# Kernel optimization log

Measured on AMD Instinct MI355X. Metric: run time of the kernel, lower is better.

Reference implementation:

```python
import jax, jax.numpy as jnp
import numpy as np

NUM_ITEMS = 200000
EMBED_DIM = 128
EPS = 1e-8  # torch cosine_similarity eps
TEMP = 0.1


def setup_inputs() -> dict:
    key = jax.random.key(0)
    k1, k2, k3, k4, k5, k6, k7, k8 = jax.random.split(key, 8)
    g1 = jax.random.normal(k1, (NUM_ITEMS, EMBED_DIM), dtype=jnp.float32)
    g2 = jax.random.normal(k2, (NUM_ITEMS, EMBED_DIM), dtype=jnp.float32)
    s1 = jax.random.normal(k3, (NUM_ITEMS, EMBED_DIM), dtype=jnp.float32)
    s2 = jax.random.normal(k4, (NUM_ITEMS, EMBED_DIM), dtype=jnp.float32)
    att_w = jax.random.normal(k5, (2 * EMBED_DIM,), dtype=jnp.float32)
    idx = jnp.arange(NUM_ITEMS, dtype=jnp.int32)
    # negative index != i, uniform over remaining items (matches resample loop)
    def neg(k):
        off = jax.random.randint(k, (NUM_ITEMS,), 1, NUM_ITEMS, dtype=jnp.int32)
        return (idx + off) % NUM_ITEMS
    return {
        "g_emb_1": g1, "g_emb_2": g2, "s_emb_1": s1, "s_emb_2": s2,
        "att_w": att_w,
        "neg_graph": neg(k6), "neg_seq": neg(k7), "neg_cross": neg(k8),
    }


def _cos(a, b):
    # rowwise cosine similarity with torch-style eps clamp on norm product
    num = jnp.sum(a * b, axis=-1)
    na = jnp.linalg.norm(a, axis=-1)
    nb = jnp.linalg.norm(b, axis=-1)
    return num / jnp.maximum(na * nb, EPS)


def _info_nce(e1, e2, neg_idx, temperature=TEMP):
    pos = _cos(e1, e2)                 # [N]
    neg = _cos(e1, e2[neg_idx])        # [N]
    # -log(exp(p/t)/(exp(p/t)+exp(n/t))) == softplus((n-p)/t)
    return jnp.mean(jax.nn.softplus((neg - pos) / temperature))


def reference(g_emb_1, g_emb_2, s_emb_1, s_emb_2, att_w,
              neg_graph, neg_seq, neg_cross):
    L_graph = _info_nce(g_emb_1, g_emb_2, neg_graph)
    L_seq = _info_nce(s_emb_1, s_emb_2, neg_seq)
    g_avg = 0.5 * (g_emb_1 + g_emb_2)
    s_avg = 0.5 * (s_emb_1 + s_emb_2)
    L_cross = _info_nce(g_avg, s_avg, neg_cross)
    L_CL = L_graph + L_seq + 1.0 * L_cross  # cross_weight = 1.0
    combined = jnp.concatenate([g_avg, s_avg], axis=1)  # [N, 2D]
    alpha = jax.nn.sigmoid(combined @ att_w)[:, None]   # [N, 1]
    item_embeddings = alpha * g_avg + (1.0 - alpha) * s_avg
    return item_embeddings, L_CL
```

## Files before the change

kernel.cpp:

```cpp
#include <hip/hip_runtime.h>

#define N_ITEMS 200000
#define EPSV 1e-8f
#define INV_TEMP 10.0f

__device__ __forceinline__ float softplus_f(float x) {
    return fmaxf(x, 0.0f) + log1pf(expf(-fabsf(x)));
}

__device__ __forceinline__ float dot8(const float4& a0, const float4& a1,
                                      const float4& b0, const float4& b1) {
    return a0.x * b0.x + a0.y * b0.y + a0.z * b0.z + a0.w * b0.w +
           a1.x * b1.x + a1.y * b1.y + a1.z * b1.z + a1.w * b1.w;
}

__device__ __forceinline__ float4 avg4(const float4& a, const float4& b) {
    return make_float4(0.5f * (a.x + b.x), 0.5f * (a.y + b.y),
                       0.5f * (a.z + b.z), 0.5f * (a.w + b.w));
}

__global__ void mvr_init_ws(float* ws) {
    if (threadIdx.x < 3) ws[threadIdx.x] = 0.0f;
}

__global__ __launch_bounds__(256) void mvr_main(
    const float* __restrict__ g1, const float* __restrict__ g2,
    const float* __restrict__ s1, const float* __restrict__ s2,
    const float* __restrict__ att_w,
    const int* __restrict__ neg_g, const int* __restrict__ neg_s,
    const int* __restrict__ neg_c,
    float* __restrict__ out, float* __restrict__ loss_acc)
{
    const int tid = threadIdx.x;
    const int lane = tid & 63;
    const int g = lane >> 4;
    const int l = lane & 15;
    const int wavesPerBlock = blockDim.x >> 6;
    const int waveId = blockIdx.x * wavesPerBlock + (tid >> 6);
    const int waveStride = gridDim.x * wavesPerBlock;

    const float4* W = (const float4*)att_w;
    const float4 wa0 = W[l], wa1 = W[16 + l];
    const float4 wb0 = W[32 + l], wb1 = W[48 + l];

    const float4* G1p = (const float4*)g1;
    const float4* G2p = (const float4*)g2;
    const float4* S1p = (const float4*)s1;
    const float4* S2p = (const float4*)s2;
    float4* Op = (float4*)out;

    float accG = 0.0f, accS = 0.0f, accC = 0.0f;

    for (int base = waveId * 4; base < N_ITEMS; base += waveStride * 4) {
        const int item = base + g;
        const size_t rb = (size_t)item * 32;

        float4 G1a = G1p[rb + l], G1b = G1p[rb + 16 + l];
        float4 G2a = G2p[rb + l], G2b = G2p[rb + 16 + l];
        float4 S1a = S1p[rb + l], S1b = S1p[rb + 16 + l];
        float4 S2a = S2p[rb + l], S2b = S2p[rb + 16 + l];

        const int jg = neg_g[item];
        const int js = neg_s[item];
        const int jc = neg_c[item];
        const size_t rg = (size_t)jg * 32, rs = (size_t)js * 32, rc = (size_t)jc * 32;
        float4 Gna = G2p[rg + l], Gnb = G2p[rg + 16 + l];
        float4 Sna = S2p[rs + l], Snb = S2p[rs + 16 + l];
        float4 C1a = S1p[rc + l], C1b = S1p[rc + 16 + l];
        float4 C2a = S2p[rc + l], C2b = S2p[rc + 16 + l];

        float4 GAa = avg4(G1a, G2a), GAb = avg4(G1b, G2b);
        float4 SAa = avg4(S1a, S2a), SAb = avg4(S1b, S2b);
        float4 CNa = avg4(C1a, C2a), CNb = avg4(C1b, C2b);

        float v[16];
        v[0]  = dot8(G1a, G1b, G2a, G2b);
        v[1]  = dot8(G1a, G1b, G1a, G1b);
        v[2]  = dot8(G2a, G2b, G2a, G2b);
        v[3]  = dot8(G1a, G1b, Gna, Gnb);
        v[4]  = dot8(Gna, Gnb, Gna, Gnb);
        v[5]  = dot8(S1a, S1b, S2a, S2b);
        v[6]  = dot8(S1a, S1b, S1a, S1b);
        v[7]  = dot8(S2a, S2b, S2a, S2b);
        v[8]  = dot8(S1a, S1b, Sna, Snb);
        v[9]  = dot8(Sna, Snb, Sna, Snb);
        v[10] = dot8(GAa, GAb, SAa, SAb);
        v[11] = dot8(GAa, GAb, GAa, GAb);
        v[12] = dot8(SAa, SAb, SAa, SAb);
        v[13] = dot8(GAa, GAb, CNa, CNb);
        v[14] = dot8(CNa, CNb, CNa, CNb);
        v[15] = dot8(GAa, GAb, wa0, wa1) + dot8(SAa, SAb, wb0, wb1);

        #pragma unroll
        for (int off = 8; off > 0; off >>= 1) {
            #pragma unroll
            for (int k = 0; k < 16; k++)
                v[k] += __shfl_xor(v[k], off, 64);
        }

        const float ng1 = sqrtf(v[1]), ng2 = sqrtf(v[2]), ngn = sqrtf(v[4]);
        const float cgp = v[0] / fmaxf(ng1 * ng2, EPSV);
        const float cgn = v[3] / fmaxf(ng1 * ngn, EPSV);
        accG += softplus_f((cgn - cgp) * INV_TEMP);

        const float ns1 = sqrtf(v[6]), ns2 = sqrtf(v[7]), nsn = sqrtf(v[9]);
        const float csp = v[5] / fmaxf(ns1 * ns2, EPSV);
        const float csn = v[8] / fmaxf(ns1 * nsn, EPSV);
        accS += softplus_f((csn - csp) * INV_TEMP);

        const float nga = sqrtf(v[11]), nsa = sqrtf(v[12]), nsan = sqrtf(v[14]);
        const float ccp = v[10] / fmaxf(nga * nsa, EPSV);
        const float ccn = v[13] / fmaxf(nga * nsan, EPSV);
        accC += softplus_f((ccn - ccp) * INV_TEMP);

        const float alpha = 1.0f / (1.0f + expf(-v[15]));
        float4 o0, o1;
        o0.x = SAa.x + alpha * (GAa.x - SAa.x);
        o0.y = SAa.y + alpha * (GAa.y - SAa.y);
        o0.z = SAa.z + alpha * (GAa.z - SAa.z);
        o0.w = SAa.w + alpha * (GAa.w - SAa.w);
        o1.x = SAb.x + alpha * (GAb.x - SAb.x);
        o1.y = SAb.y + alpha * (GAb.y - SAb.y);
        o1.z = SAb.z + alpha * (GAb.z - SAb.z);
        o1.w = SAb.w + alpha * (GAb.w - SAb.w);
        Op[rb + l] = o0;
        Op[rb + 16 + l] = o1;
    }

    accG += __shfl_xor(accG, 16, 64); accG += __shfl_xor(accG, 32, 64);
    accS += __shfl_xor(accS, 16, 64); accS += __shfl_xor(accS, 32, 64);
    accC += __shfl_xor(accC, 16, 64); accC += __shfl_xor(accC, 32, 64);

    __shared__ float sh[4][3];
    const int wave = tid >> 6;
    if (lane == 0) {
        sh[wave][0] = accG;
        sh[wave][1] = accS;
        sh[wave][2] = accC;
    }
    __syncthreads();
    if (tid == 0) {
        float a = 0.0f, b = 0.0f, c = 0.0f;
        for (int w = 0; w < wavesPerBlock; w++) {
            a += sh[w][0]; b += sh[w][1]; c += sh[w][2];
        }
        atomicAdd(&loss_acc[0], a);
        atomicAdd(&loss_acc[1], b);
        atomicAdd(&loss_acc[2], c);
    }
}

__global__ void mvr_finalize(const float* __restrict__ loss_acc,
                             float* __restrict__ out_scalar) {
    if (threadIdx.x == 0) {
        out_scalar[0] = (loss_acc[0] + loss_acc[1] + loss_acc[2]) * (1.0f / (float)N_ITEMS);
    }
}

extern "C" void kernel_launch(void* const* d_in, const int* in_sizes, int n_in,
                              void* d_out, int out_size, void* d_ws, size_t ws_size,
                              hipStream_t stream) {
    const float* g1    = (const float*)d_in[0];
    const float* g2    = (const float*)d_in[1];
    const float* s1    = (const float*)d_in[2];
    const float* s2    = (const float*)d_in[3];
    const float* att_w = (const float*)d_in[4];
    const int*   neg_g = (const int*)d_in[5];
    const int*   neg_s = (const int*)d_in[6];
    const int*   neg_c = (const int*)d_in[7];
    float* out = (float*)d_out;
    float* ws  = (float*)d_ws;

    mvr_init_ws<<<1, 64, 0, stream>>>(ws);
    mvr_main<<<3125, 256, 0, stream>>>(g1, g2, s1, s2, att_w,
                                       neg_g, neg_s, neg_c, out, ws);
    mvr_finalize<<<1, 64, 0, stream>>>(ws, out + (size_t)N_ITEMS * 128);
}
```

Before: 460.2 us.

## Use one-item-per-wave-group grid, nontemporal loads/stores, and spread loss atomics

Replaces the grid-stride loop with a launch of 12500 blocks so that each 16-lane group handles exactly one item, and hoists the negative-index loads to the top of the kernel. The g1 loads and the output stores become nontemporal, so data read or written only once does not pollute cache that the gathered g2/s1/s2 rows could reuse. Loss atomics are spread over 16 slots to cut contention, and launch bounds gain an occupancy hint. The grid now depends on N being a multiple of 16, and there are many more blocks, each with per-block reduction overhead.

```diff
diff --git a/kernel.cpp b/kernel.cpp
--- a/kernel.cpp
+++ b/kernel.cpp
@@ -3,6 +3,7 @@
 #define N_ITEMS 200000
 #define EPSV 1e-8f
 #define INV_TEMP 10.0f
+#define NSLOT 16
 
 __device__ __forceinline__ float softplus_f(float x) {
     return fmaxf(x, 0.0f) + log1pf(expf(-fabsf(x)));
@@ -19,11 +20,21 @@
                        0.5f * (a.z + b.z), 0.5f * (a.w + b.w));
 }
 
-__global__ void mvr_init_ws(float* ws) {
-    if (threadIdx.x < 3) ws[threadIdx.x] = 0.0f;
+typedef float f32x4 __attribute__((ext_vector_type(4)));
+__device__ __forceinline__ float4 ldnt4(const float4* p) {
+    f32x4 t = __builtin_nontemporal_load((const f32x4*)p);
+    return make_float4(t.x, t.y, t.z, t.w);
+}
+__device__ __forceinline__ void stnt4(float4* p, const float4& v) {
+    f32x4 t = {v.x, v.y, v.z, v.w};
+    __builtin_nontemporal_store(t, (f32x4*)p);
 }
 
-__global__ __launch_bounds__(256) void mvr_main(
+__global__ void mvr_init_ws(float* ws) {
+    if (threadIdx.x < NSLOT * 4) ws[threadIdx.x] = 0.0f;
+}
+
+__global__ __launch_bounds__(256, 6) void mvr_main(
     const float* __restrict__ g1, const float* __restrict__ g2,
     const float* __restrict__ s1, const float* __restrict__ s2,
     const float* __restrict__ att_w,
@@ -35,13 +46,14 @@
     const int lane = tid & 63;
     const int g = lane >> 4;
     const int l = lane & 15;
-    const int wavesPerBlock = blockDim.x >> 6;
-    const int waveId = blockIdx.x * wavesPerBlock + (tid >> 6);
-    const int waveStride = gridDim.x * wavesPerBlock;
+    const int waveId = (blockIdx.x << 2) + (tid >> 6);
+    const int item = (waveId << 2) + g;
 
-    const float4* W = (const float4*)att_w;
-    const float4 wa0 = W[l], wa1 = W[16 + l];
-    const float4 wb0 = W[32 + l], wb1 = W[48 + l];
+    const int jg = neg_g[item];
+    const int js = neg_s[item];
+    const int jc = neg_c[item];
+
+    const size_t rb = (size_t)item * 32;
 
     const float4* G1p = (const float4*)g1;
     const float4* G2p = (const float4*)g2;
@@ -49,83 +61,77 @@
     const float4* S2p = (const float4*)s2;
     float4* Op = (float4*)out;
 
-    float accG = 0.0f, accS = 0.0f, accC = 0.0f;
+    float4 G1a = ldnt4(&G1p[rb + l]), G1b = ldnt4(&G1p[rb + 16 + l]);
+    float4 G2a = G2p[rb + l], G2b = G2p[rb + 16 + l];
+    float4 S1a = S1p[rb + l], S1b = S1p[rb + 16 + l];
+    float4 S2a = S2p[rb + l], S2b = S2p[rb + 16 + l];
 
-    for (int base = waveId * 4; base < N_ITEMS; base += waveStride * 4) {
-        const int item = base + g;
-        const size_t rb = (size_t)item * 32;
+    const size_t rg = (size_t)jg * 32, rs = (size_t)js * 32, rc = (size_t)jc * 32;
+    float4 Gna = G2p[rg + l], Gnb = G2p[rg + 16 + l];
+    float4 Sna = S2p[rs + l], Snb = S2p[rs + 16 + l];
+    float4 C1a = S1p[rc + l], C1b = S1p[rc + 16 + l];
+    float4 C2a = S2p[rc + l], C2b = S2p[rc + 16 + l];
 
-        float4 G1a = G1p[rb + l], G1b = G1p[rb + 16 + l];
-        float4 G2a = G2p[rb + l], G2b = G2p[rb + 16 + l];
-        float4 S1a = S1p[rb + l], S1b = S1p[rb + 16 + l];
-        float4 S2a = S2p[rb + l], S2b = S2p[rb + 16 + l];
+    const float4* W = (const float4*)att_w;
+    const float4 wa0 = W[l], wa1 = W[16 + l];
+    const float4 wb0 = W[32 + l], wb1 = W[48 + l];
 
-        const int jg = neg_g[item];
-        const int js = neg_s[item];
-        const int jc = neg_c[item];
-        const size_t rg = (size_t)jg * 32, rs = (size_t)js * 32, rc = (size_t)jc * 32;
-        float4 Gna = G2p[rg + l], Gnb = G2p[rg + 16 + l];
-        float4 Sna = S2p[rs + l], Snb = S2p[rs + 16 + l];
-        float4 C1a = S1p[rc + l], C1b = S1p[rc + 16 + l];
-        float4 C2a = S2p[rc + l], C2b = S2p[rc + 16 + l];
+    float4 GAa = avg4(G1a, G2a), GAb = avg4(G1b, G2b);
+    float4 SAa = avg4(S1a, S2a), SAb = avg4(S1b, S2b);
+    float4 CNa = avg4(C1a, C2a), CNb = avg4(C1b, C2b);
 
-        float4 GAa = avg4(G1a, G2a), GAb = avg4(G1b, G2b);
-        float4 SAa = avg4(S1a, S2a), SAb = avg4(S1b, S2b);
-        float4 CNa = avg4(C1a, C2a), CNb = avg4(C1b, C2b);
+    float v[16];
+    v[0]  = dot8(G1a, G1b, G2a, G2b);
+    v[1]  = dot8(G1a, G1b, G1a, G1b);
+    v[2]  = dot8(G2a, G2b, G2a, G2b);
+    v[3]  = dot8(G1a, G1b, Gna, Gnb);
+    v[4]  = dot8(Gna, Gnb, Gna, Gnb);
+    v[5]  = dot8(S1a, S1b, S2a, S2b);
+    v[6]  = dot8(S1a, S1b, S1a, S1b);
+    v[7]  = dot8(S2a, S2b, S2a, S2b);
+    v[8]  = dot8(S1a, S1b, Sna, Snb);
+    v[9]  = dot8(Sna, Snb, Sna, Snb);
+    v[10] = dot8(GAa, GAb, SAa, SAb);
+    v[11] = dot8(GAa, GAb, GAa, GAb);
+    v[12] = dot8(SAa, SAb, SAa, SAb);
+    v[13] = dot8(GAa, GAb, CNa, CNb);
+    v[14] = dot8(CNa, CNb, CNa, CNb);
+    v[15] = dot8(GAa, GAb, wa0, wa1) + dot8(SAa, SAb, wb0, wb1);
 
-        float v[16];
-        v[0]  = dot8(G1a, G1b, G2a, G2b);
-        v[1]  = dot8(G1a, G1b, G1a, G1b);
-        v[2]  = dot8(G2a, G2b, G2a, G2b);
-        v[3]  = dot8(G1a, G1b, Gna, Gnb);
-        v[4]  = dot8(Gna, Gnb, Gna, Gnb);
-        v[5]  = dot8(S1a, S1b, S2a, S2b);
-        v[6]  = dot8(S1a, S1b, S1a, S1b);
-        v[7]  = dot8(S2a, S2b, S2a, S2b);
-        v[8]  = dot8(S1a, S1b, Sna, Snb);
-        v[9]  = dot8(Sna, Snb, Sna, Snb);
-        v[10] = dot8(GAa, GAb, SAa, SAb);
-        v[11] = dot8(GAa, GAb, GAa, GAb);
-        v[12] = dot8(SAa, SAb, SAa, SAb);
-        v[13] = dot8(GAa, GAb, CNa, CNb);
-        v[14] = dot8(CNa, CNb, CNa, CNb);
-        v[15] = dot8(GAa, GAb, wa0, wa1) + dot8(SAa, SAb, wb0, wb1);
+    #pragma unroll
+    for (int off = 8; off > 0; off >>= 1) {
+        #pragma unroll
+        for (int k = 0; k < 16; k++)
+            v[k] += __shfl_xor(v[k], off, 64);
+    }
 
-        #pragma unroll
-        for (int off = 8; off > 0; off >>= 1) {
-            #pragma unroll
-            for (int k = 0; k < 16; k++)
-                v[k] += __shfl_xor(v[k], off, 64);
-        }
+    const float ng1 = sqrtf(v[1]), ng2 = sqrtf(v[2]), ngn = sqrtf(v[4]);
+    const float cgp = v[0] / fmaxf(ng1 * ng2, EPSV);
+    const float cgn = v[3] / fmaxf(ng1 * ngn, EPSV);
+    float accG = softplus_f((cgn - cgp) * INV_TEMP);
 
-        const float ng1 = sqrtf(v[1]), ng2 = sqrtf(v[2]), ngn = sqrtf(v[4]);
-        const float cgp = v[0] / fmaxf(ng1 * ng2, EPSV);
-        const float cgn = v[3] / fmaxf(ng1 * ngn, EPSV);
-        accG += softplus_f((cgn - cgp) * INV_TEMP);
+    const float ns1 = sqrtf(v[6]), ns2 = sqrtf(v[7]), nsn = sqrtf(v[9]);
+    const float csp = v[5] / fmaxf(ns1 * ns2, EPSV);
+    const float csn = v[8] / fmaxf(ns1 * nsn, EPSV);
+    float accS = softplus_f((csn - csp) * INV_TEMP);
 
-        const float ns1 = sqrtf(v[6]), ns2 = sqrtf(v[7]), nsn = sqrtf(v[9]);
-        const float csp = v[5] / fmaxf(ns1 * ns2, EPSV);
-        const float csn = v[8] / fmaxf(ns1 * nsn, EPSV);
-        accS += softplus_f((csn - csp) * INV_TEMP);
+    const float nga = sqrtf(v[11]), nsa = sqrtf(v[12]), nsan = sqrtf(v[14]);
+    const float ccp = v[10] / fmaxf(nga * nsa, EPSV);
+    const float ccn = v[13] / fmaxf(nga * nsan, EPSV);
+    float accC = softplus_f((ccn - ccp) * INV_TEMP);
 
-        const float nga = sqrtf(v[11]), nsa = sqrtf(v[12]), nsan = sqrtf(v[14]);
-        const float ccp = v[10] / fmaxf(nga * nsa, EPSV);
-        const float ccn = v[13] / fmaxf(nga * nsan, EPSV);
-        accC += softplus_f((ccn - ccp) * INV_TEMP);
-
-        const float alpha = 1.0f / (1.0f + expf(-v[15]));
-        float4 o0, o1;
-        o0.x = SAa.x + alpha * (GAa.x - SAa.x);
-        o0.y = SAa.y + alpha * (GAa.y - SAa.y);
-        o0.z = SAa.z + alpha * (GAa.z - SAa.z);
-        o0.w = SAa.w + alpha * (GAa.w - SAa.w);
-        o1.x = SAb.x + alpha * (GAb.x - SAb.x);
-        o1.y = SAb.y + alpha * (GAb.y - SAb.y);
-        o1.z = SAb.z + alpha * (GAb.z - SAb.z);
-        o1.w = SAb.w + alpha * (GAb.w - SAb.w);
-        Op[rb + l] = o0;
-        Op[rb + 16 + l] = o1;
-    }
+    const float alpha = 1.0f / (1.0f + expf(-v[15]));
+    float4 o0, o1;
+    o0.x = SAa.x + alpha * (GAa.x - SAa.x);
+    o0.y = SAa.y + alpha * (GAa.y - SAa.y);
+    o0.z = SAa.z + alpha * (GAa.z - SAa.z);
+    o0.w = SAa.w + alpha * (GAa.w - SAa.w);
+    o1.x = SAb.x + alpha * (GAb.x - SAb.x);
+    o1.y = SAb.y + alpha * (GAb.y - SAb.y);
+    o1.z = SAb.z + alpha * (GAb.z - SAb.z);
+    o1.w = SAb.w + alpha * (GAb.w - SAb.w);
+    stnt4(&Op[rb + l], o0);
+    stnt4(&Op[rb + 16 + l], o1);
 
     accG += __shfl_xor(accG, 16, 64); accG += __shfl_xor(accG, 32, 64);
     accS += __shfl_xor(accS, 16, 64); accS += __shfl_xor(accS, 32, 64);
@@ -141,19 +147,24 @@
     __syncthreads();
     if (tid == 0) {
         float a = 0.0f, b = 0.0f, c = 0.0f;
-        for (int w = 0; w < wavesPerBlock; w++) {
+        #pragma unroll
+        for (int w = 0; w < 4; w++) {
             a += sh[w][0]; b += sh[w][1]; c += sh[w][2];
         }
-        atomicAdd(&loss_acc[0], a);
-        atomicAdd(&loss_acc[1], b);
-        atomicAdd(&loss_acc[2], c);
+        const int slot = (blockIdx.x & (NSLOT - 1)) * 4;
+        atomicAdd(&loss_acc[slot + 0], a);
+        atomicAdd(&loss_acc[slot + 1], b);
+        atomicAdd(&loss_acc[slot + 2], c);
     }
 }
 
 __global__ void mvr_finalize(const float* __restrict__ loss_acc,
                              float* __restrict__ out_scalar) {
     if (threadIdx.x == 0) {
-        out_scalar[0] = (loss_acc[0] + loss_acc[1] + loss_acc[2]) * (1.0f / (float)N_ITEMS);
+        float t = 0.0f;
+        for (int s = 0; s < NSLOT; s++)
+            t += loss_acc[s * 4 + 0] + loss_acc[s * 4 + 1] + loss_acc[s * 4 + 2];
+        out_scalar[0] = t * (1.0f / (float)N_ITEMS);
     }
 }
 
@@ -172,7 +183,7 @@
     float* ws  = (float*)d_ws;
 
     mvr_init_ws<<<1, 64, 0, stream>>>(ws);
-    mvr_main<<<3125, 256, 0, stream>>>(g1, g2, s1, s2, att_w,
-                                       neg_g, neg_s, neg_c, out, ws);
+    mvr_main<<<12500, 256, 0, stream>>>(g1, g2, s1, s2, att_w,
+                                        neg_g, neg_s, neg_c, out, ws);
     mvr_finalize<<<1, 64, 0, stream>>>(ws, out + (size_t)N_ITEMS * 128);
 }
```

New measurement: 524.5 us. 14.0% more time.
